# Performance work log

Hardware: AMD Instinct MI355X
Metric: run time of the kernel (lower is better)

The kernel has to match this reference:

```python
import jax, jax.numpy as jnp
import numpy as np

N_NODES = 100000
IN_C = 300
OUT_C = 200
N_EDGES = 1600000
NEG_SLOPE = 0.2  # PyG GATConv default


def setup_inputs() -> dict:
    key = jax.random.key(0)
    ks = jax.random.split(key, 12)
    x = jax.random.normal(ks[0], (N_NODES, IN_C), dtype=jnp.float32)
    edge_index = jax.random.randint(ks[1], (2, N_EDGES), 0, N_NODES, dtype=jnp.int64)
    s0 = 1.0 / np.sqrt(IN_C)
    s1 = 1.0 / np.sqrt(OUT_C)
    return {
        "x": x,
        "W0": jax.random.normal(ks[2], (IN_C, OUT_C), dtype=jnp.float32) * s0,
        "a_src0": jax.random.normal(ks[3], (OUT_C,), dtype=jnp.float32) * s1,
        "a_dst0": jax.random.normal(ks[4], (OUT_C,), dtype=jnp.float32) * s1,
        "b0": jnp.zeros((OUT_C,), dtype=jnp.float32),
        "W1": jax.random.normal(ks[5], (OUT_C, OUT_C), dtype=jnp.float32) * s1,
        "a_src1": jax.random.normal(ks[6], (OUT_C,), dtype=jnp.float32) * s1,
        "a_dst1": jax.random.normal(ks[7], (OUT_C,), dtype=jnp.float32) * s1,
        "b1": jnp.zeros((OUT_C,), dtype=jnp.float32),
        "edge_index": edge_index,
    }


def _gat_conv(x, W, a_src, a_dst, b, src, dst, n):
    # h: [N, F'] projected features
    h = x @ W
    alpha_src = h @ a_src  # [N]
    alpha_dst = h @ a_dst  # [N]
    # per-edge raw attention score, message flows src -> dst
    e = jax.nn.leaky_relu(alpha_src[src] + alpha_dst[dst], NEG_SLOPE)  # [E]
    # segment softmax over incoming edges of each destination node
    m = jax.ops.segment_max(e, dst, num_segments=n)
    ex = jnp.exp(e - m[dst])
    denom = jax.ops.segment_sum(ex, dst, num_segments=n)
    alpha = ex / denom[dst]  # [E]
    # scatter-add weighted messages
    out = jax.ops.segment_sum(h[src] * alpha[:, None], dst, num_segments=n)
    return out + b


def reference(x, W0, a_src0, a_dst0, b0, W1, a_src1, a_dst1, b1, edge_index):
    n = x.shape[0]
    # PyG GATConv default: add self-loops
    loops = jnp.arange(n, dtype=edge_index.dtype)
    src = jnp.concatenate([edge_index[0], loops])
    dst = jnp.concatenate([edge_index[1], loops])
    h = jax.nn.relu(_gat_conv(x, W0, a_src0, a_dst0, b0, src, dst, n))
    h = jax.nn.relu(_gat_conv(h, W1, a_src1, a_dst1, b1, src, dst, n))
    return h
```

## Files before the change

kernel.cpp:

```cpp
#include <hip/hip_runtime.h>

#define IN_C 300
#define OUT_C 200
#define NEG_SLOPE 0.2f

#define BMB 128
#define BMW 16
#define BKC 20

static inline int cdiv(long a, int b) { return (int)((a + b - 1) / b); }

__device__ __forceinline__ void glds16(const float* g, float* l) {
  __builtin_amdgcn_global_load_lds(
      (const __attribute__((address_space(1))) void*)g,
      (__attribute__((address_space(3))) void*)l, 16, 0, 0);
}

__global__ __launch_bounds__(256)
void zero_int_kernel(int* __restrict__ p, int n) {
  int i = blockIdx.x * blockDim.x + threadIdx.x;
  if (i < n) p[i] = 0;
}

__device__ __forceinline__ void edge_sd(const int* __restrict__ src,
                                        const int* __restrict__ dst,
                                        int i, int E, int& s, int& d) {
  if (i < E) { s = src[i]; d = dst[i]; } else { s = d = i - E; }
}

__global__ __launch_bounds__(256)
void padw_kernel(const float* __restrict__ W, float* __restrict__ Wpad, int K) {
  int idx = blockIdx.x * blockDim.x + threadIdx.x;
  if (idx >= K * 64) return;
  int k = idx >> 6, c = (idx & 63) * 4;
  float4 v = make_float4(0.f, 0.f, 0.f, 0.f);
  if (c < OUT_C) v = *(const float4*)(W + (long)k * OUT_C + c);
  *(float4*)(Wpad + (long)k * 256 + c) = v;
}

__global__ __launch_bounds__(256)
void hist_kernel(const int* __restrict__ src, const int* __restrict__ dst,
                 int E, int ET, int* __restrict__ counts) {
  int i = blockIdx.x * blockDim.x + threadIdx.x;
  if (i >= ET) return;
  int s, d; edge_sd(src, dst, i, E, s, d);
  atomicAdd(counts + d, 1);
}

__global__ __launch_bounds__(256)
void scan_a_kernel(const int* __restrict__ in, int n, int* __restrict__ out,
                   int* __restrict__ bsums) {
  __shared__ int lds[256];
  int t = threadIdx.x;
  int base = blockIdx.x * 1024 + t * 4;
  int v0 = (base + 0 < n) ? in[base + 0] : 0;
  int v1 = (base + 1 < n) ? in[base + 1] : 0;
  int v2 = (base + 2 < n) ? in[base + 2] : 0;
  int v3 = (base + 3 < n) ? in[base + 3] : 0;
  int s1 = v0 + v1, s2 = s1 + v2, s3 = s2 + v3;
  lds[t] = s3;
  __syncthreads();
  for (int o = 1; o < 256; o <<= 1) {
    int x = (t >= o) ? lds[t - o] : 0;
    __syncthreads();
    lds[t] += x;
    __syncthreads();
  }
  int pre = (t > 0) ? lds[t - 1] : 0;
  if (base + 0 < n) out[base + 0] = pre + v0;
  if (base + 1 < n) out[base + 1] = pre + s1;
  if (base + 2 < n) out[base + 2] = pre + s2;
  if (base + 3 < n) out[base + 3] = pre + s3;
  if (t == 255) bsums[blockIdx.x] = lds[255];
}

__global__ __launch_bounds__(256)
void scan_b_kernel(int* __restrict__ bs, int nb) {
  __shared__ int lds[256];
  int t = threadIdx.x;
  lds[t] = (t < nb) ? bs[t] : 0;
  __syncthreads();
  for (int o = 1; o < 256; o <<= 1) {
    int x = (t >= o) ? lds[t - o] : 0;
    __syncthreads();
    lds[t] += x;
    __syncthreads();
  }
  if (t < nb) bs[t] = lds[t];
}

__global__ __launch_bounds__(256)
void scan_c_kernel(int* __restrict__ out, int n, const int* __restrict__ bs) {
  int i = blockIdx.x * blockDim.x + threadIdx.x;
  if (i >= n) return;
  int b = i >> 10;
  if (b > 0) out[i] += bs[b - 1];
}

__global__ __launch_bounds__(256)
void fill_kernel(const int* __restrict__ src, const int* __restrict__ dst,
                 int E, int ET, const int* __restrict__ rowptr,
                 int* __restrict__ cursor, int* __restrict__ csr_src) {
  int i = blockIdx.x * blockDim.x + threadIdx.x;
  if (i >= ET) return;
  int s, d; edge_sd(src, dst, i, E, s, d);
  int pos = rowptr[d] + atomicAdd(cursor + d, 1);
  csr_src[pos] = s;
}

__global__ __launch_bounds__(512)
void gemm_ws_kernel(const float* __restrict__ A, const float* __restrict__ Wpad,
                    const float* __restrict__ a_src, const float* __restrict__ a_dst,
                    float* __restrict__ H, float* __restrict__ asN,
                    float* __restrict__ adN, int K, int N) {
  __shared__ float Ws[2][BKC][256];
  __shared__ float As[2][BMB][BKC];
  int t = threadIdx.x;
  int wave = t >> 6, lane = t & 63;
  int col = lane * 4;
  long row0 = (long)blockIdx.x * BMB;
  int wrow = wave * BMW;

  const float* sW = Wpad + (long)wave * 256 + col;
  int f0 = t;
  long ar0 = row0 + f0 / 5; if (ar0 >= N) ar0 = N - 1;
  const float* sA0 = A + ar0 * K + (f0 % 5) * 4;
  int f1 = 512 + t;
  long ar1 = row0 + f1 / 5; if (ar1 >= N) ar1 = N - 1;
  const float* sA1 = A + ar1 * K + (f1 % 5) * 4;

  auto stage = [&](int buf) {
    #pragma unroll
    for (int j = 0; j < 3; ++j) {
      int r = wave + j * 8;
      if (r < BKC) glds16(sW + j * 8 * 256, &Ws[buf][r][0]);
    }
    glds16(sA0, &As[buf][0][0] + wave * 256);
    if (t < 128) glds16(sA1, &As[buf][0][0] + 2048 + wave * 256);
    sW += BKC * 256; sA0 += BKC; sA1 += BKC;
  };

  float4 acc[BMW];
  #pragma unroll
  for (int r = 0; r < BMW; ++r) acc[r] = make_float4(0.f, 0.f, 0.f, 0.f);

  const int nch = K / BKC;
  stage(0);
  int cur = 0;
  for (int ch = 0; ch < nch; ++ch) {
    __syncthreads();
    if (ch + 1 < nch) stage(cur ^ 1);
    #pragma unroll
    for (int kk = 0; kk < BKC; kk += 4) {
      float4 w0 = *(float4*)&Ws[cur][kk + 0][col];
      float4 w1 = *(float4*)&Ws[cur][kk + 1][col];
      float4 w2 = *(float4*)&Ws[cur][kk + 2][col];
      float4 w3 = *(float4*)&Ws[cur][kk + 3][col];
      #pragma unroll
      for (int r = 0; r < BMW; ++r) {
        float4 a = *(float4*)&As[cur][wrow + r][kk];
        acc[r].x = fmaf(a.x, w0.x, acc[r].x);
        acc[r].x = fmaf(a.y, w1.x, acc[r].x);
        acc[r].x = fmaf(a.z, w2.x, acc[r].x);
        acc[r].x = fmaf(a.w, w3.x, acc[r].x);
        acc[r].y = fmaf(a.x, w0.y, acc[r].y);
        acc[r].y = fmaf(a.y, w1.y, acc[r].y);
        acc[r].y = fmaf(a.z, w2.y, acc[r].y);
        acc[r].y = fmaf(a.w, w3.y, acc[r].y);
        acc[r].z = fmaf(a.x, w0.z, acc[r].z);
        acc[r].z = fmaf(a.y, w1.z, acc[r].z);
        acc[r].z = fmaf(a.z, w2.z, acc[r].z);
        acc[r].z = fmaf(a.w, w3.z, acc[r].z);
        acc[r].w = fmaf(a.x, w0.w, acc[r].w);
        acc[r].w = fmaf(a.y, w1.w, acc[r].w);
        acc[r].w = fmaf(a.z, w2.w, acc[r].w);
        acc[r].w = fmaf(a.w, w3.w, acc[r].w);
      }
    }
    cur ^= 1;
  }

  bool cok = col < OUT_C;
  #pragma unroll
  for (int r = 0; r < BMW; ++r) {
    long grow = row0 + wrow + r;
    if (cok && grow < N) *(float4*)(H + grow * OUT_C + col) = acc[r];
  }
  float4 vs = make_float4(0.f, 0.f, 0.f, 0.f);
  float4 vd = make_float4(0.f, 0.f, 0.f, 0.f);
  if (cok) {
    vs = *(const float4*)(a_src + col);
    vd = *(const float4*)(a_dst + col);
  }
  #pragma unroll
  for (int r = 0; r < BMW; ++r) {
    float ss = acc[r].x * vs.x + acc[r].y * vs.y + acc[r].z * vs.z + acc[r].w * vs.w;
    float sd = acc[r].x * vd.x + acc[r].y * vd.y + acc[r].z * vd.z + acc[r].w * vd.w;
    #pragma unroll
    for (int o = 32; o > 0; o >>= 1) {
      ss += __shfl_xor(ss, o);
      sd += __shfl_xor(sd, o);
    }
    long grow = row0 + wrow + r;
    if (lane == 0 && grow < N) { asN[grow] = ss; adN[grow] = sd; }
  }
}

__global__ __launch_bounds__(256)
void gather_agg_kernel(const float* __restrict__ h, const float* __restrict__ asN,
                       const float* __restrict__ adN, const int* __restrict__ rowptr,
                       const int* __restrict__ csr_src, const float* __restrict__ bias,
                       float* __restrict__ out, int N) {
  int wid = (int)(((long)blockIdx.x * blockDim.x + threadIdx.x) >> 6);
  int lane = threadIdx.x & 63;
  if (wid >= N) return;
  int start = rowptr[wid], end = rowptr[wid + 1];
  float ad = adN[wid];
  int c = lane * 4;
  bool cok = c < OUT_C;
  const float* hc = h + c;

  float4 acc = make_float4(0.f, 0.f, 0.f, 0.f);
  float se = 0.f;
  int j = start;
  for (; j + 2 <= end; j += 2) {
    int s0 = csr_src[j], s1 = csr_src[j + 1];
    float e0 = asN[s0] + ad, e1 = asN[s1] + ad;
    e0 = e0 > 0.f ? e0 : NEG_SLOPE * e0;
    e1 = e1 > 0.f ? e1 : NEG_SLOPE * e1;
    float w0 = __expf(e0), w1 = __expf(e1);
    se += w0 + w1;
    if (cok) {
      float4 h0 = *(const float4*)(hc + (long)s0 * OUT_C);
      float4 h1 = *(const float4*)(hc + (long)s1 * OUT_C);
      acc.x = fmaf(w0, h0.x, acc.x); acc.x = fmaf(w1, h1.x, acc.x);
      acc.y = fmaf(w0, h0.y, acc.y); acc.y = fmaf(w1, h1.y, acc.y);
      acc.z = fmaf(w0, h0.z, acc.z); acc.z = fmaf(w1, h1.z, acc.z);
      acc.w = fmaf(w0, h0.w, acc.w); acc.w = fmaf(w1, h1.w, acc.w);
    }
  }
  if (j < end) {
    int s0 = csr_src[j];
    float e0 = asN[s0] + ad;
    e0 = e0 > 0.f ? e0 : NEG_SLOPE * e0;
    float w0 = __expf(e0);
    se += w0;
    if (cok) {
      float4 h0 = *(const float4*)(hc + (long)s0 * OUT_C);
      acc.x = fmaf(w0, h0.x, acc.x);
      acc.y = fmaf(w0, h0.y, acc.y);
      acc.z = fmaf(w0, h0.z, acc.z);
      acc.w = fmaf(w0, h0.w, acc.w);
    }
  }
  if (cok) {
    float inv = 1.0f / se;
    float4 bv = *(const float4*)(bias + c);
    float4 o;
    o.x = fmaxf(fmaf(acc.x, inv, bv.x), 0.f);
    o.y = fmaxf(fmaf(acc.y, inv, bv.y), 0.f);
    o.z = fmaxf(fmaf(acc.z, inv, bv.z), 0.f);
    o.w = fmaxf(fmaf(acc.w, inv, bv.w), 0.f);
    *(float4*)(out + (long)wid * OUT_C + c) = o;
  }
}

static void run_layer(const float* xin, int K, const float* Wpad,
                      const float* a_s, const float* a_d, const float* b,
                      const int* rowptr, const int* csr_src, int N,
                      float* hbuf, float* asN, float* adN, float* outbuf,
                      hipStream_t stream) {
  gemm_ws_kernel<<<cdiv(N, BMB), 512, 0, stream>>>(xin, Wpad, a_s, a_d,
                                                   hbuf, asN, adN, K, N);
  gather_agg_kernel<<<cdiv((long)N * 64, 256), 256, 0, stream>>>(
      hbuf, asN, adN, rowptr, csr_src, b, outbuf, N);
}

extern "C" void kernel_launch(void* const* d_in, const int* in_sizes, int n_in,
                              void* d_out, int out_size, void* d_ws, size_t ws_size,
                              hipStream_t stream) {
  const float* x   = (const float*)d_in[0];
  const float* W0  = (const float*)d_in[1];
  const float* as0 = (const float*)d_in[2];
  const float* ad0 = (const float*)d_in[3];
  const float* b0  = (const float*)d_in[4];
  const float* W1  = (const float*)d_in[5];
  const float* as1 = (const float*)d_in[6];
  const float* ad1 = (const float*)d_in[7];
  const float* b1  = (const float*)d_in[8];
  const int*   ei  = (const int*)d_in[9];

  const int N  = in_sizes[0] / IN_C;
  const int E  = in_sizes[9] / 2;
  const int ET = E + N;
  const int* src = ei;
  const int* dst = ei + E;

  float* out = (float*)d_out;

  char* ws = (char*)d_ws;
  float* hbuf   = (float*)ws;
  float* asN    = (float*)(ws + (size_t)N * OUT_C * 4);
  float* adN    = asN + N;
  int*   rowptr = (int*)(adN + N);
  int*   counts = rowptr + (N + 1);
  int*   bsums  = counts + N;
  int*   csrsrc = bsums + 256;
  size_t woff = ((size_t)(csrsrc + ET - (int*)ws) + 3) & ~(size_t)3;
  float* wpad0 = (float*)ws + woff;
  float* wpad1 = wpad0 + (size_t)IN_C * 256;

  const int nb = cdiv(N, 1024);

  padw_kernel<<<cdiv(IN_C * 64, 256), 256, 0, stream>>>(W0, wpad0, IN_C);
  padw_kernel<<<cdiv(OUT_C * 64, 256), 256, 0, stream>>>(W1, wpad1, OUT_C);
  zero_int_kernel<<<cdiv(N, 256), 256, 0, stream>>>(counts, N);
  hist_kernel<<<cdiv(ET, 256), 256, 0, stream>>>(src, dst, E, ET, counts);
  scan_a_kernel<<<nb, 256, 0, stream>>>(counts, N, rowptr + 1, bsums);
  scan_b_kernel<<<1, 256, 0, stream>>>(bsums, nb);
  scan_c_kernel<<<cdiv(N, 256), 256, 0, stream>>>(rowptr + 1, N, bsums);
  zero_int_kernel<<<1, 256, 0, stream>>>(rowptr, 1);
  zero_int_kernel<<<cdiv(N, 256), 256, 0, stream>>>(counts, N);
  fill_kernel<<<cdiv(ET, 256), 256, 0, stream>>>(src, dst, E, ET, rowptr, counts, csrsrc);

  run_layer(x, IN_C, wpad0, as0, ad0, b0, rowptr, csrsrc, N, hbuf, asN, adN, out, stream);
  run_layer(out, OUT_C, wpad1, as1, ad1, b1, rowptr, csrsrc, N, hbuf, asN, adN, out, stream);
}
```

Measured before the change: 1.213 ms.

## Drop W padding kernels, stage W via registers, halve GEMM block, unroll gather by four

Removes the two padding kernels and loads the unpadded W chunk into registers, writing it to a single shared buffer each chunk. GEMM blocks shrink to 64 rows and 256 threads to raise occupancy. The gather loop is unrolled to four edges so more feature loads are in flight. The single W buffer needs an extra barrier per chunk. Lanes near the end of a row read W columns past 200 (spilling into the next row or uninitialized shared memory), which is only harmless if those columns are never stored.

```diff
diff --git a/kernel.cpp b/kernel.cpp
--- a/kernel.cpp
+++ b/kernel.cpp
@@ -4,9 +4,10 @@
 #define OUT_C 200
 #define NEG_SLOPE 0.2f
 
-#define BMB 128
+#define BMB 64
 #define BMW 16
 #define BKC 20
+#define WF4 1000
 
 static inline int cdiv(long a, int b) { return (int)((a + b - 1) / b); }
 
@@ -26,16 +27,6 @@
                                         const int* __restrict__ dst,
                                         int i, int E, int& s, int& d) {
   if (i < E) { s = src[i]; d = dst[i]; } else { s = d = i - E; }
-}
-
-__global__ __launch_bounds__(256)
-void padw_kernel(const float* __restrict__ W, float* __restrict__ Wpad, int K) {
-  int idx = blockIdx.x * blockDim.x + threadIdx.x;
-  if (idx >= K * 64) return;
-  int k = idx >> 6, c = (idx & 63) * 4;
-  float4 v = make_float4(0.f, 0.f, 0.f, 0.f);
-  if (c < OUT_C) v = *(const float4*)(W + (long)k * OUT_C + c);
-  *(float4*)(Wpad + (long)k * 256 + c) = v;
 }
 
 __global__ __launch_bounds__(256)
@@ -108,12 +99,12 @@
   csr_src[pos] = s;
 }
 
-__global__ __launch_bounds__(512)
-void gemm_ws_kernel(const float* __restrict__ A, const float* __restrict__ Wpad,
+__global__ __launch_bounds__(256)
+void gemm_ws_kernel(const float* __restrict__ A, const float* __restrict__ W,
                     const float* __restrict__ a_src, const float* __restrict__ a_dst,
                     float* __restrict__ H, float* __restrict__ asN,
                     float* __restrict__ adN, int K, int N) {
-  __shared__ float Ws[2][BKC][256];
+  __shared__ float Wf[4096];
   __shared__ float As[2][BMB][BKC];
   int t = threadIdx.x;
   int wave = t >> 6, lane = t & 63;
@@ -121,23 +112,32 @@
   long row0 = (long)blockIdx.x * BMB;
   int wrow = wave * BMW;
 
-  const float* sW = Wpad + (long)wave * 256 + col;
+  const bool pw3ok = t < (WF4 - 768);
+  float4 pw0, pw1, pw2, pw3;
+  const float* wsrc = W;
+  auto loadW = [&]() {
+    pw0 = *(const float4*)(wsrc + t * 4);
+    pw1 = *(const float4*)(wsrc + 1024 + t * 4);
+    pw2 = *(const float4*)(wsrc + 2048 + t * 4);
+    if (pw3ok) pw3 = *(const float4*)(wsrc + 3072 + t * 4);
+    wsrc += BKC * OUT_C;
+  };
+  auto writeW = [&]() {
+    float4* wf4 = (float4*)Wf;
+    wf4[t] = pw0; wf4[256 + t] = pw1; wf4[512 + t] = pw2;
+    if (pw3ok) wf4[768 + t] = pw3;
+  };
+
   int f0 = t;
   long ar0 = row0 + f0 / 5; if (ar0 >= N) ar0 = N - 1;
   const float* sA0 = A + ar0 * K + (f0 % 5) * 4;
-  int f1 = 512 + t;
+  int f1 = 256 + t;
   long ar1 = row0 + f1 / 5; if (ar1 >= N) ar1 = N - 1;
   const float* sA1 = A + ar1 * K + (f1 % 5) * 4;
-
-  auto stage = [&](int buf) {
-    #pragma unroll
-    for (int j = 0; j < 3; ++j) {
-      int r = wave + j * 8;
-      if (r < BKC) glds16(sW + j * 8 * 256, &Ws[buf][r][0]);
-    }
-    glds16(sA0, &As[buf][0][0] + wave * 256);
-    if (t < 128) glds16(sA1, &As[buf][0][0] + 2048 + wave * 256);
-    sW += BKC * 256; sA0 += BKC; sA1 += BKC;
+  auto loadA = [&](int buf) {
+    glds16(sA0, (float*)As[buf] + wave * 256);
+    if (t < 64) glds16(sA1, (float*)As[buf] + 1024);
+    sA0 += BKC; sA1 += BKC;
   };
 
   float4 acc[BMW];
@@ -145,17 +145,20 @@
   for (int r = 0; r < BMW; ++r) acc[r] = make_float4(0.f, 0.f, 0.f, 0.f);
 
   const int nch = K / BKC;
-  stage(0);
+  loadW();
+  loadA(0);
   int cur = 0;
   for (int ch = 0; ch < nch; ++ch) {
     __syncthreads();
-    if (ch + 1 < nch) stage(cur ^ 1);
+    writeW();
+    __syncthreads();
+    if (ch + 1 < nch) { loadW(); loadA(cur ^ 1); }
     #pragma unroll
     for (int kk = 0; kk < BKC; kk += 4) {
-      float4 w0 = *(float4*)&Ws[cur][kk + 0][col];
-      float4 w1 = *(float4*)&Ws[cur][kk + 1][col];
-      float4 w2 = *(float4*)&Ws[cur][kk + 2][col];
-      float4 w3 = *(float4*)&Ws[cur][kk + 3][col];
+      float4 w0 = *(float4*)&Wf[(kk + 0) * OUT_C + col];
+      float4 w1 = *(float4*)&Wf[(kk + 1) * OUT_C + col];
+      float4 w2 = *(float4*)&Wf[(kk + 2) * OUT_C + col];
+      float4 w3 = *(float4*)&Wf[(kk + 3) * OUT_C + col];
       #pragma unroll
       for (int r = 0; r < BMW; ++r) {
         float4 a = *(float4*)&As[cur][wrow + r][kk];
@@ -223,23 +226,33 @@
   float4 acc = make_float4(0.f, 0.f, 0.f, 0.f);
   float se = 0.f;
   int j = start;
-  for (; j + 2 <= end; j += 2) {
+  for (; j + 4 <= end; j += 4) {
     int s0 = csr_src[j], s1 = csr_src[j + 1];
+    int s2 = csr_src[j + 2], s3 = csr_src[j + 3];
     float e0 = asN[s0] + ad, e1 = asN[s1] + ad;
+    float e2 = asN[s2] + ad, e3 = asN[s3] + ad;
     e0 = e0 > 0.f ? e0 : NEG_SLOPE * e0;
     e1 = e1 > 0.f ? e1 : NEG_SLOPE * e1;
-    float w0 = __expf(e0), w1 = __expf(e1);
-    se += w0 + w1;
+    e2 = e2 > 0.f ? e2 : NEG_SLOPE * e2;
+    e3 = e3 > 0.f ? e3 : NEG_SLOPE * e3;
+    float w0 = __expf(e0), w1 = __expf(e1), w2 = __expf(e2), w3 = __expf(e3);
+    se += (w0 + w1) + (w2 + w3);
     if (cok) {
       float4 h0 = *(const float4*)(hc + (long)s0 * OUT_C);
       float4 h1 = *(const float4*)(hc + (long)s1 * OUT_C);
+      float4 h2 = *(const float4*)(hc + (long)s2 * OUT_C);
+      float4 h3 = *(const float4*)(hc + (long)s3 * OUT_C);
       acc.x = fmaf(w0, h0.x, acc.x); acc.x = fmaf(w1, h1.x, acc.x);
+      acc.x = fmaf(w2, h2.x, acc.x); acc.x = fmaf(w3, h3.x, acc.x);
       acc.y = fmaf(w0, h0.y, acc.y); acc.y = fmaf(w1, h1.y, acc.y);
+      acc.y = fmaf(w2, h2.y, acc.y); acc.y = fmaf(w3, h3.y, acc.y);
       acc.z = fmaf(w0, h0.z, acc.z); acc.z = fmaf(w1, h1.z, acc.z);
+      acc.z = fmaf(w2, h2.z, acc.z); acc.z = fmaf(w3, h3.z, acc.z);
       acc.w = fmaf(w0, h0.w, acc.w); acc.w = fmaf(w1, h1.w, acc.w);
+      acc.w = fmaf(w2, h2.w, acc.w); acc.w = fmaf(w3, h3.w, acc.w);
     }
   }
-  if (j < end) {
+  for (; j < end; ++j) {
     int s0 = csr_src[j];
     float e0 = asN[s0] + ad;
     e0 = e0 > 0.f ? e0 : NEG_SLOPE * e0;
@@ -265,12 +278,12 @@
   }
 }
 
-static void run_layer(const float* xin, int K, const float* Wpad,
+static void run_layer(const float* xin, int K, const float* W,
                       const float* a_s, const float* a_d, const float* b,
                       const int* rowptr, const int* csr_src, int N,
                       float* hbuf, float* asN, float* adN, float* outbuf,
                       hipStream_t stream) {
-  gemm_ws_kernel<<<cdiv(N, BMB), 512, 0, stream>>>(xin, Wpad, a_s, a_d,
+  gemm_ws_kernel<<<cdiv(N, BMB), 256, 0, stream>>>(xin, W, a_s, a_d,
                                                    hbuf, asN, adN, K, N);
   gather_agg_kernel<<<cdiv((long)N * 64, 256), 256, 0, stream>>>(
       hbuf, asN, adN, rowptr, csr_src, b, outbuf, N);
@@ -306,14 +319,9 @@
   int*   counts = rowptr + (N + 1);
   int*   bsums  = counts + N;
   int*   csrsrc = bsums + 256;
-  size_t woff = ((size_t)(csrsrc + ET - (int*)ws) + 3) & ~(size_t)3;
-  float* wpad0 = (float*)ws + woff;
-  float* wpad1 = wpad0 + (size_t)IN_C * 256;
 
   const int nb = cdiv(N, 1024);
 
-  padw_kernel<<<cdiv(IN_C * 64, 256), 256, 0, stream>>>(W0, wpad0, IN_C);
-  padw_kernel<<<cdiv(OUT_C * 64, 256), 256, 0, stream>>>(W1, wpad1, OUT_C);
   zero_int_kernel<<<cdiv(N, 256), 256, 0, stream>>>(counts, N);
   hist_kernel<<<cdiv(ET, 256), 256, 0, stream>>>(src, dst, E, ET, counts);
   scan_a_kernel<<<nb, 256, 0, stream>>>(counts, N, rowptr + 1, bsums);
@@ -323,6 +331,6 @@
   zero_int_kernel<<<cdiv(N, 256), 256, 0, stream>>>(counts, N);
   fill_kernel<<<cdiv(ET, 256), 256, 0, stream>>>(src, dst, E, ET, rowptr, counts, csrsrc);
 
-  run_layer(x, IN_C, wpad0, as0, ad0, b0, rowptr, csrsrc, N, hbuf, asN, adN, out, stream);
-  run_layer(out, OUT_C, wpad1, as1, ad1, b1, rowptr, csrsrc, N, hbuf, asN, adN, out, stream);
-}
+  run_layer(x, IN_C, W0, as0, ad0, b0, rowptr, csrsrc, N, hbuf, asN, adN, out, stream);
+  run_layer(out, OUT_C, W1, as1, ad1, b1, rowptr, csrsrc, N, hbuf, asN, adN, out, stream);
+}
```

After: 1.116 ms. -8.0%, faster.
